# Kernel optimization log

Hardware: AMD Instinct MI355X
Metric: run time of the kernel (lower is better)

Reference implementation:

```python
import jax, jax.numpy as jnp
import numpy as np

B, T, D = 2048, 60, 6
H, F, O = 64, 10, 1


def setup_inputs() -> dict:
    key = jax.random.key(0)
    ks = jax.random.split(key, 16)
    w = lambda k, shape, s=0.1: jax.random.normal(k, shape, jnp.float32) * s
    return {
        "x": jax.random.normal(ks[0], (B, T, D), jnp.float32),
        "W_i": w(ks[1], (D, H)), "U_i": w(ks[2], (H, H)), "b_i": jnp.zeros((H,), jnp.float32),
        "W_ste": w(ks[3], (D, H)), "U_ste": w(ks[4], (H, H)), "b_ste": jnp.ones((H,), jnp.float32),
        "W_fre": w(ks[5], (D, F)), "U_fre": w(ks[6], (H, F)), "b_fre": jnp.ones((F,), jnp.float32),
        "W_c": w(ks[7], (D, H)), "U_c": w(ks[8], (H, H)), "b_c": jnp.zeros((H,), jnp.float32),
        "W_o": w(ks[9], (D, H)), "U_o": w(ks[10], (H, H)), "b_o": jnp.zeros((H,), jnp.float32),
        "U_a": w(ks[11], (F, 1)), "b_a": jnp.zeros((H,), jnp.float32),
        "W_p": w(ks[12], (H, O)), "b_p": jnp.zeros((O,), jnp.float32),
    }


def _hsig(v):
    # torch.nn.Hardsigmoid: relu6(x + 3) / 6
    return jnp.clip(v / 6.0 + 0.5, 0.0, 1.0)


def reference(x, W_i, U_i, b_i, W_ste, U_ste, b_ste, W_fre, U_fre, b_fre,
              W_c, U_c, b_c, W_o, U_o, b_o, U_a, b_a, W_p, b_p):
    b, t_len, _ = x.shape
    h_dim = W_i.shape[1]
    f_dim = W_fre.shape[1]
    freq = jnp.arange(f_dim, dtype=x.dtype) / f_dim  # (F,)
    ua = U_a[:, 0]  # (F,)

    def step(carry, x_t):
        h, S_re, S_im, t = carry
        i = _hsig(x_t @ W_i + b_i + h @ U_i)              # (B,H)
        ste = _hsig(x_t @ W_ste + b_ste + h @ U_ste)      # (B,H)
        fre = _hsig(x_t @ W_fre + b_fre + h @ U_fre)      # (B,F)
        f = ste[:, :, None] * fre[:, None, :]             # (B,H,F)
        c = i * jnp.tanh(x_t @ W_c + b_c + h @ U_c)       # (B,H)
        t = t + 1.0
        omega = (2.0 * jnp.pi) * t * freq                  # (F,)
        S_re = f * S_re + c[:, :, None] * jnp.cos(omega)   # (B,H,F)
        S_im = f * S_im + c[:, :, None] * jnp.sin(omega)   # (B,H,F)
        A = S_re * S_re + S_im * S_im                      # (B,H,F)
        a = jnp.tanh(jnp.einsum('bhf,f->bh', A, ua) + b_a)
        o = _hsig(x_t @ W_o + b_o + h @ U_o)
        h = o * a
        return (h, S_re, S_im, t), None

    init = (jnp.zeros((b, h_dim), x.dtype),
            jnp.zeros((b, h_dim, f_dim), x.dtype),
            jnp.zeros((b, h_dim, f_dim), x.dtype),
            jnp.asarray(0.0, x.dtype))
    (h, _, _, _), _ = jax.lax.scan(step, init, jnp.swapaxes(x, 0, 1))
    # original returns p from the last timestep only
    return h @ W_p + b_p
```

## Files before the change

kernel.cpp:

```cpp
#include <hip/hip_runtime.h>


#define BB 2048
#define TT 60
#define DD 6
#define HH 64
#define FF 10
#define NB 8

#define XS 968
#define HSK 72

typedef short bf16x8 __attribute__((ext_vector_type(8)));
typedef float f32x4  __attribute__((ext_vector_type(4)));

__device__ __forceinline__ unsigned short f2bf(float f) {
    union { float f; unsigned u; } v; v.f = f;
    unsigned r = v.u + 0x7fffu + ((v.u >> 16) & 1u);
    return (unsigned short)(r >> 16);
}
__device__ __forceinline__ float bf2f(unsigned short b) {
    union { unsigned u; float f; } v; v.u = ((unsigned)b) << 16; return v.f;
}
__device__ __forceinline__ float hsig_f(float v) {
    return __builtin_amdgcn_fmed3f(fmaf(v, 0.16666666666666666f, 0.5f), 0.0f, 1.0f);
}
__device__ __forceinline__ float tanh_f(float x) {
    float xc = fminf(fmaxf(x, -12.0f), 12.0f);
    float e  = __builtin_amdgcn_exp2f(xc * 2.8853900817779268f);
    return (e - 1.0f) * __builtin_amdgcn_rcpf(e + 1.0f);
}
__device__ __forceinline__ float uni(float v) {
    return __int_as_float(__builtin_amdgcn_readfirstlane(__float_as_int(v)));
}
__device__ __forceinline__ void pinv(bf16x8& v) { asm volatile("" : "+v"(v)); }

__global__ __launch_bounds__(256)
__attribute__((amdgpu_waves_per_eu(1, 1)))
void sfm_kernel(
    const float* __restrict__ x,
    const float* __restrict__ W_i,  const float* __restrict__ U_i,  const float* __restrict__ b_i,
    const float* __restrict__ W_ste,const float* __restrict__ U_ste,const float* __restrict__ b_ste,
    const float* __restrict__ W_fre,const float* __restrict__ U_fre,const float* __restrict__ b_fre,
    const float* __restrict__ W_c,  const float* __restrict__ U_c,  const float* __restrict__ b_c,
    const float* __restrict__ W_o,  const float* __restrict__ U_o,  const float* __restrict__ b_o,
    const float* __restrict__ U_a,  const float* __restrict__ b_a,
    const float* __restrict__ W_p,  const float* __restrict__ b_p,
    float* __restrict__ out)
{
    const int tid  = threadIdx.x;
    const int lane = tid & 63;
    const int wave = tid >> 6;
    const int q    = lane >> 4;
    const int n16  = lane & 15;
    const int b0   = blockIdx.x * NB;

    __shared__ __align__(16) unsigned short xsp[NB * XS];
    __shared__ __align__(16) unsigned short hsp2[16 * HSK];
    __shared__ __align__(16) float fbw[4][8][16];
    __shared__ __align__(16) float ctab[10 * 10 * 2];
    __shared__ float cstabB[10 * 2];
    __shared__ float red[4][NB];

    for (int item = tid; item < NB * TT; item += 256) {
        const float* xg = x + (size_t)b0 * (TT * DD) + item * DD;
        const int b = item / TT, s = item - b * TT;
        unsigned short* dst = &xsp[b * XS + s * 16];
        #pragma unroll
        for (int d = 0; d < DD; ++d) {
            const float v = xg[d];
            const unsigned short hb = f2bf(v);
            dst[d]     = hb;
            dst[8 + d] = f2bf(v - bf2f(hb));
        }
        dst[6] = 0x3F80; dst[7] = 0;
        dst[14] = 0; dst[15] = 0;
    }
    if (tid < 10) {
        const float CTc[10] = { 1.0f,  0.8090169943749475f,  0.30901699437494745f,
                               -0.30901699437494745f, -0.8090169943749475f, -1.0f,
                               -0.8090169943749475f, -0.30901699437494745f,
                                0.30901699437494745f,  0.8090169943749475f };
        const float STc[10] = { 0.0f,  0.5877852522924731f,  0.9510565162951535f,
                                0.9510565162951535f,  0.5877852522924731f,  0.0f,
                               -0.5877852522924731f, -0.9510565162951535f,
                               -0.9510565162951535f, -0.5877852522924731f };
        float cc = 0.0f, ss = 0.0f;
        #pragma unroll
        for (int j = 0; j < 10; ++j) if (tid == j) { cc = CTc[j]; ss = STc[j]; }
        cstabB[tid * 2] = cc; cstabB[tid * 2 + 1] = ss;
    }
    for (int i = tid; i < 16 * HSK; i += 256) hsp2[i] = 0;
    __syncthreads();
    if (tid < 100) {
        const int mm = tid / 10, ff = tid - mm * 10;
        const int idx = (ff * mm) % 10;
        ctab[tid * 2]     = cstabB[idx * 2];
        ctab[tid * 2 + 1] = cstabB[idx * 2 + 1];
    }

    bf16x8 Ah[5][3], Al[5][3];
    #pragma unroll
    for (int t = 0; t < 5; ++t) {
        const float* Up = (t==0)?U_i:(t==1)?U_ste:(t==2)?U_c:(t==3)?U_o:U_fre;
        const float* Wp = (t==0)?W_i:(t==1)?W_ste:(t==2)?W_c:(t==3)?W_o:W_fre;
        const float* bp = (t==0)?b_i:(t==1)?b_ste:(t==2)?b_c:(t==3)?b_o:b_fre;
        const int nd  = (t < 4) ? HH : FF;
        const int col = (t < 4) ? (wave * 16 + n16) : n16;
        const bool ok = (t < 4) || (n16 < FF);
        #pragma unroll
        for (int c = 0; c < 3; ++c) {
            #pragma unroll
            for (int j = 0; j < 8; ++j) {
                const int kv = c * 32 + q * 8 + j;
                float v = 0.0f;
                if (ok) {
                    if      (kv < 64)  v = Up[kv * nd + col];
                    else if (kv < 70)  v = Wp[(kv - 64) * nd + col];
                    else if (kv == 70) v = bp[col];
                }
                const unsigned short hb = f2bf(v);
                Ah[t][c][j] = (short)hb;
                Al[t][c][j] = (short)f2bf(v - bf2f(hb));
            }
            pinv(Ah[t][c]); pinv(Al[t][c]);
        }
    }

    const int b   = n16 & 7;
    const int hi3 = n16 >> 3;
    const int hc0 = wave * 16 + q * 4 + hi3 * 2;
    const float ba0 = b_a[hc0], ba1 = b_a[hc0 + 1];
    const float wp0 = W_p[hc0], wp1 = W_p[hc0 + 1];
    const float bpv = uni(b_p[0]);
    float uav[FF];
    #pragma unroll
    for (int f = 0; f < FF; ++f) uav[f] = uni(U_a[f]);

    float Sre0[FF], Sim0[FF], Sre1[FF], Sim1[FF];
    #pragma unroll
    for (int f = 0; f < FF; ++f) { Sre0[f]=0.f; Sim0[f]=0.f; Sre1[f]=0.f; Sim1[f]=0.f; }
    float hv0 = 0.0f, hv1 = 0.0f;

    const unsigned short* hrp = &hsp2[n16 * HSK];
    const unsigned short* xrp = &xsp[b * XS + hi3 * 8];

    __syncthreads();

    int m = 1;
    for (int s = 0; s < TT; ++s) {
        const bf16x8 B0 = *(const bf16x8*)&hrp[q * 8];
        const bf16x8 B1 = *(const bf16x8*)&hrp[32 + q * 8];
        const bf16x8 xv = *(const bf16x8*)&xrp[s * 16];
        const bf16x8 zf8 = {0, 0, 0, 0, 0, 0, 0, 0};
        const bf16x8 B2 = (q == 0) ? xv : zf8;

        f32x4 acc[5];
        #pragma unroll
        for (int t = 0; t < 5; ++t) {
            f32x4 a = {0.0f, 0.0f, 0.0f, 0.0f};
            a = __builtin_amdgcn_mfma_f32_16x16x32_bf16(Ah[t][0], B0, a, 0, 0, 0);
            a = __builtin_amdgcn_mfma_f32_16x16x32_bf16(Al[t][0], B0, a, 0, 0, 0);
            a = __builtin_amdgcn_mfma_f32_16x16x32_bf16(Ah[t][1], B1, a, 0, 0, 0);
            a = __builtin_amdgcn_mfma_f32_16x16x32_bf16(Al[t][1], B1, a, 0, 0, 0);
            a = __builtin_amdgcn_mfma_f32_16x16x32_bf16(Ah[t][2], B2, a, 0, 0, 0);
            a = __builtin_amdgcn_mfma_f32_16x16x32_bf16(Al[t][2], B2, a, 0, 0, 0);
            acc[t] = a;
        }

        f32x4 z[5];
        #pragma unroll
        for (int t = 0; t < 5; ++t) {
            #pragma unroll
            for (int r = 0; r < 4; ++r)
                z[t][r] = acc[t][r] + __shfl_xor(acc[t][r], 8, 64);
        }

        if (n16 < 8) *(f32x4*)&fbw[wave][n16][q * 4] = z[4];
        asm volatile("" ::: "memory");
        const f32x4  fA = *(const f32x4*)&fbw[wave][b][0];
        const f32x4  fB = *(const f32x4*)&fbw[wave][b][4];
        const float2 fC = *(const float2*)&fbw[wave][b][8];
        float fr[FF];
        #pragma unroll
        for (int f = 0; f < 4; ++f) fr[f] = hsig_f(fA[f]);
        #pragma unroll
        for (int f = 0; f < 4; ++f) fr[4 + f] = hsig_f(fB[f]);
        fr[8] = hsig_f(fC.x); fr[9] = hsig_f(fC.y);

        const float zi0 = hi3 ? z[0][2] : z[0][0], zi1 = hi3 ? z[0][3] : z[0][1];
        const float zs0 = hi3 ? z[1][2] : z[1][0], zs1 = hi3 ? z[1][3] : z[1][1];
        const float zc0 = hi3 ? z[2][2] : z[2][0], zc1 = hi3 ? z[2][3] : z[2][1];
        const float zo0 = hi3 ? z[3][2] : z[3][0], zo1 = hi3 ? z[3][3] : z[3][1];

        const float iv0 = hsig_f(zi0), st0 = hsig_f(zs0), ov0 = hsig_f(zo0);
        const float iv1 = hsig_f(zi1), st1 = hsig_f(zs1), ov1 = hsig_f(zo1);
        const float cv0 = iv0 * tanh_f(zc0);
        const float cv1 = iv1 * tanh_f(zc1);

        const float* tp = &ctab[m * 20];
        float a00 = ba0, a01 = 0.0f, a10 = ba1, a11 = 0.0f;
        #pragma unroll
        for (int f = 0; f < FF; ++f) {
            const float2 tv = *(const float2*)&tp[f * 2];
            const float fc0 = st0 * fr[f];
            const float fc1 = st1 * fr[f];
            Sre0[f] = fmaf(fc0, Sre0[f], cv0 * tv.x);
            Sim0[f] = fmaf(fc0, Sim0[f], cv0 * tv.y);
            Sre1[f] = fmaf(fc1, Sre1[f], cv1 * tv.x);
            Sim1[f] = fmaf(fc1, Sim1[f], cv1 * tv.y);
            const float A0 = fmaf(Sim0[f], Sim0[f], Sre0[f] * Sre0[f]);
            const float A1 = fmaf(Sim1[f], Sim1[f], Sre1[f] * Sre1[f]);
            if (f & 1) { a01 = fmaf(A0, uav[f], a01); a11 = fmaf(A1, uav[f], a11); }
            else       { a00 = fmaf(A0, uav[f], a00); a10 = fmaf(A1, uav[f], a10); }
        }
        hv0 = ov0 * tanh_f(a00 + a01);
        hv1 = ov1 * tanh_f(a10 + a11);

        {
            const unsigned short hA = f2bf(hv0);
            const unsigned short hB = f2bf(hv1);
            hsp2[b * HSK + hc0]           = hA;
            hsp2[(8 + b) * HSK + hc0]     = f2bf(hv0 - bf2f(hA));
            hsp2[b * HSK + hc0 + 1]       = hB;
            hsp2[(8 + b) * HSK + hc0 + 1] = f2bf(hv1 - bf2f(hB));
        }
        if (++m == 10) m = 0;
        __syncthreads();
    }

    float val = fmaf(hv0, wp0, hv1 * wp1);
    val += __shfl_xor(val, 8, 64);
    val += __shfl_xor(val, 16, 64);
    val += __shfl_xor(val, 32, 64);
    if (lane < 8) red[wave][lane] = val;
    __syncthreads();
    if (tid < NB)
        out[b0 + tid] = red[0][tid] + red[1][tid] + red[2][tid] + red[3][tid] + bpv;
}

extern "C" void kernel_launch(void* const* d_in, const int* in_sizes, int n_in,
                              void* d_out, int out_size, void* d_ws, size_t ws_size,
                              hipStream_t stream) {
    (void)in_sizes; (void)n_in; (void)d_ws; (void)ws_size; (void)out_size;
    const float* x     = (const float*)d_in[0];
    const float* W_i   = (const float*)d_in[1];
    const float* U_i   = (const float*)d_in[2];
    const float* b_i   = (const float*)d_in[3];
    const float* W_ste = (const float*)d_in[4];
    const float* U_ste = (const float*)d_in[5];
    const float* b_ste = (const float*)d_in[6];
    const float* W_fre = (const float*)d_in[7];
    const float* U_fre = (const float*)d_in[8];
    const float* b_fre = (const float*)d_in[9];
    const float* W_c   = (const float*)d_in[10];
    const float* U_c   = (const float*)d_in[11];
    const float* b_c   = (const float*)d_in[12];
    const float* W_o   = (const float*)d_in[13];
    const float* U_o   = (const float*)d_in[14];
    const float* b_o   = (const float*)d_in[15];
    const float* U_a   = (const float*)d_in[16];
    const float* b_a   = (const float*)d_in[17];
    const float* W_p   = (const float*)d_in[18];
    const float* b_p   = (const float*)d_in[19];

    sfm_kernel<<<BB / NB, 256, 0, stream>>>(
        x, W_i, U_i, b_i, W_ste, U_ste, b_ste, W_fre, U_fre, b_fre,
        W_c, U_c, b_c, W_o, U_o, b_o, U_a, b_a, W_p, b_p, (float*)d_out);
}
```

Before: 160.6 us.

## Halve batch rows per block and allow two waves per EU

```diff
diff --git a/kernel.cpp b/kernel.cpp
--- a/kernel.cpp
+++ b/kernel.cpp
@@ -6,7 +6,7 @@
 #define DD 6
 #define HH 64
 #define FF 10
-#define NB 8
+#define NB 4
 
 #define XS 968
 #define HSK 72
@@ -35,8 +35,7 @@
 }
 __device__ __forceinline__ void pinv(bf16x8& v) { asm volatile("" : "+v"(v)); }
 
-__global__ __launch_bounds__(256)
-__attribute__((amdgpu_waves_per_eu(1, 1)))
+__global__ __launch_bounds__(256, 2)
 void sfm_kernel(
     const float* __restrict__ x,
     const float* __restrict__ W_i,  const float* __restrict__ U_i,  const float* __restrict__ b_i,
@@ -57,14 +56,14 @@
 
     __shared__ __align__(16) unsigned short xsp[NB * XS];
     __shared__ __align__(16) unsigned short hsp2[16 * HSK];
-    __shared__ __align__(16) float fbw[4][8][16];
+    __shared__ __align__(16) float fbw[4][4][16];
     __shared__ __align__(16) float ctab[10 * 10 * 2];
     __shared__ float cstabB[10 * 2];
     __shared__ float red[4][NB];
 
-    for (int item = tid; item < NB * TT; item += 256) {
-        const float* xg = x + (size_t)b0 * (TT * DD) + item * DD;
-        const int b = item / TT, s = item - b * TT;
+    if (tid < NB * TT) {
+        const float* xg = x + (size_t)b0 * (TT * DD) + tid * DD;
+        const int b = tid / TT, s = tid - b * TT;
         unsigned short* dst = &xsp[b * XS + s * 16];
         #pragma unroll
         for (int d = 0; d < DD; ++d) {
@@ -127,9 +126,10 @@
         }
     }
 
-    const int b   = n16 & 7;
-    const int hi3 = n16 >> 3;
-    const int hc0 = wave * 16 + q * 4 + hi3 * 2;
+    const int  b     = n16 & 3;
+    const int  copy  = (n16 >> 2) & 1;
+    const bool valid = (n16 < 8);
+    const int  hc0   = wave * 16 + q * 4 + copy * 2;
     const float ba0 = b_a[hc0], ba1 = b_a[hc0 + 1];
     const float wp0 = W_p[hc0], wp1 = W_p[hc0 + 1];
     const float bpv = uni(b_p[0]);
@@ -143,7 +143,7 @@
     float hv0 = 0.0f, hv1 = 0.0f;
 
     const unsigned short* hrp = &hsp2[n16 * HSK];
-    const unsigned short* xrp = &xsp[b * XS + hi3 * 8];
+    const unsigned short* xrp = &xsp[b * XS + copy * 8];
 
     __syncthreads();
 
@@ -153,7 +153,7 @@
         const bf16x8 B1 = *(const bf16x8*)&hrp[32 + q * 8];
         const bf16x8 xv = *(const bf16x8*)&xrp[s * 16];
         const bf16x8 zf8 = {0, 0, 0, 0, 0, 0, 0, 0};
-        const bf16x8 B2 = (q == 0) ? xv : zf8;
+        const bf16x8 B2 = (q == 0 && valid) ? xv : zf8;
 
         f32x4 acc[5];
         #pragma unroll
@@ -173,10 +173,10 @@
         for (int t = 0; t < 5; ++t) {
             #pragma unroll
             for (int r = 0; r < 4; ++r)
-                z[t][r] = acc[t][r] + __shfl_xor(acc[t][r], 8, 64);
-        }
-
-        if (n16 < 8) *(f32x4*)&fbw[wave][n16][q * 4] = z[4];
+                z[t][r] = acc[t][r] + __shfl_xor(acc[t][r], 4, 64);
+        }
+
+        if (n16 < 4) *(f32x4*)&fbw[wave][n16][q * 4] = z[4];
         asm volatile("" ::: "memory");
         const f32x4  fA = *(const f32x4*)&fbw[wave][b][0];
         const f32x4  fB = *(const f32x4*)&fbw[wave][b][4];
@@ -188,10 +188,10 @@
         for (int f = 0; f < 4; ++f) fr[4 + f] = hsig_f(fB[f]);
         fr[8] = hsig_f(fC.x); fr[9] = hsig_f(fC.y);
 
-        const float zi0 = hi3 ? z[0][2] : z[0][0], zi1 = hi3 ? z[0][3] : z[0][1];
-        const float zs0 = hi3 ? z[1][2] : z[1][0], zs1 = hi3 ? z[1][3] : z[1][1];
-        const float zc0 = hi3 ? z[2][2] : z[2][0], zc1 = hi3 ? z[2][3] : z[2][1];
-        const float zo0 = hi3 ? z[3][2] : z[3][0], zo1 = hi3 ? z[3][3] : z[3][1];
+        const float zi0 = copy ? z[0][2] : z[0][0], zi1 = copy ? z[0][3] : z[0][1];
+        const float zs0 = copy ? z[1][2] : z[1][0], zs1 = copy ? z[1][3] : z[1][1];
+        const float zc0 = copy ? z[2][2] : z[2][0], zc1 = copy ? z[2][3] : z[2][1];
+        const float zo0 = copy ? z[3][2] : z[3][0], zo1 = copy ? z[3][3] : z[3][1];
 
         const float iv0 = hsig_f(zi0), st0 = hsig_f(zs0), ov0 = hsig_f(zo0);
         const float iv1 = hsig_f(zi1), st1 = hsig_f(zs1), ov1 = hsig_f(zo1);
@@ -217,23 +217,23 @@
         hv0 = ov0 * tanh_f(a00 + a01);
         hv1 = ov1 * tanh_f(a10 + a11);
 
-        {
+        if (valid) {
             const unsigned short hA = f2bf(hv0);
             const unsigned short hB = f2bf(hv1);
             hsp2[b * HSK + hc0]           = hA;
-            hsp2[(8 + b) * HSK + hc0]     = f2bf(hv0 - bf2f(hA));
+            hsp2[(4 + b) * HSK + hc0]     = f2bf(hv0 - bf2f(hA));
             hsp2[b * HSK + hc0 + 1]       = hB;
-            hsp2[(8 + b) * HSK + hc0 + 1] = f2bf(hv1 - bf2f(hB));
+            hsp2[(4 + b) * HSK + hc0 + 1] = f2bf(hv1 - bf2f(hB));
         }
         if (++m == 10) m = 0;
         __syncthreads();
     }
 
-    float val = fmaf(hv0, wp0, hv1 * wp1);
-    val += __shfl_xor(val, 8, 64);
+    float val = valid ? fmaf(hv0, wp0, hv1 * wp1) : 0.0f;
+    val += __shfl_xor(val, 4, 64);
     val += __shfl_xor(val, 16, 64);
     val += __shfl_xor(val, 32, 64);
-    if (lane < 8) red[wave][lane] = val;
+    if (lane < NB) red[wave][lane] = val;
     __syncthreads();
     if (tid < NB)
         out[b0 + tid] = red[0][tid] + red[1][tid] + red[2][tid] + red[3][tid] + bpv;
```

Measured after the change: 181.9 us. 13.3% more time.
